# Kernel tuning notes

Measured on AMD Instinct MI355X. Metric: run time of the kernel, lower is better.

Reference implementation:

```python
import jax, jax.numpy as jnp
import numpy as np

LAMBDA = 25.0
MU = 25.0
NU = 1.0
ALPHA = 0.25
EPS = 1e-4
NUM_MATCHES = (20, 4)


def _cdist(x, y):
    # x: (B, L1, C), y: (B, L2, C) -> (B, L1, L2) euclidean distances
    x2 = jnp.sum(x * x, axis=-1)[..., :, None]
    y2 = jnp.sum(y * y, axis=-1)[..., None, :]
    d2 = x2 + y2 - 2.0 * jnp.einsum('blc,bmc->blm', x, y)
    return jnp.sqrt(jnp.maximum(d2, 0.0))


def _nearest_neighbors(input_maps, candidate_maps, distances, num_matches):
    # For each input location, its nearest candidate; then keep the
    # num_matches input locations with smallest NN distance, in original order.
    nn_dist = jnp.min(distances, axis=-1)    # (B, L1)
    nn_idx = jnp.argmin(distances, axis=-1)  # (B, L1)
    _, sel = jax.lax.top_k(-nn_dist, num_matches)  # (B, M) smallest distances
    sel = jnp.sort(sel, axis=1)  # restore original ordering of positions
    filtered_input = jnp.take_along_axis(input_maps, sel[..., None], axis=1)
    nn_sel = jnp.take_along_axis(nn_idx, sel, axis=1)
    filtered_candidate = jnp.take_along_axis(candidate_maps, nn_sel[..., None], axis=1)
    return filtered_input, filtered_candidate


def _mse(a, b):
    return jnp.mean((a - b) ** 2)


def _vicreg_loss(z_a, z_b):
    inv_loss = _mse(z_a, z_b)

    def var_loss(z):
        std = jnp.sqrt(jnp.var(z, axis=0, ddof=1) + EPS)
        return jnp.mean(jax.nn.relu(1.0 - std))

    def cov_loss(z):
        n, d = z.shape
        zc = z - jnp.mean(z, axis=0)
        cov = (zc.T @ zc) / (n - 1)
        off = cov - jnp.diag(jnp.diag(cov))
        return jnp.sum(off ** 2) / d

    v = 0.5 * (var_loss(z_a) + var_loss(z_b))
    c = cov_loss(z_a) + cov_loss(z_b)
    return LAMBDA * inv_loss + MU * v + NU * c


def _local_loss(z_global, z_local, grid_global, grid_local):
    B = z_global.shape[0]
    zg = z_global.reshape(B, -1, z_global.shape[-1])   # (B, Lg, C)
    zl = z_local.reshape(B, -1, z_local.shape[-1])     # (B, Ll, C)

    inv_loss = 0.0
    # feature-space NN
    gf, gn = _nearest_neighbors(zg, zl, _cdist(zg, zl), NUM_MATCHES[0])
    lf, ln = _nearest_neighbors(zl, zg, _cdist(zl, zg), NUM_MATCHES[1])
    inv_loss = inv_loss + (_mse(gf, gn) / 2 + _mse(lf, ln) / 2)

    # grid-space NN (distances from grids, gather from feature maps)
    gg = grid_global.reshape(B, -1, 2)
    gl = grid_local.reshape(B, -1, 2)
    gf, gn = _nearest_neighbors(zg, zl, _cdist(gg, gl), NUM_MATCHES[0])
    lf, ln = _nearest_neighbors(zl, zg, _cdist(gl, gg), NUM_MATCHES[1])
    inv_loss = inv_loss + (_mse(gf, gn) / 2 + _mse(lf, ln) / 2)

    return LAMBDA * inv_loss


def setup_inputs() -> dict:
    key = jax.random.key(0)
    ks = jax.random.split(key, 6)
    B, D, C = 32, 8192, 512
    return {
        'z_global': jax.random.normal(ks[0], (B, D), jnp.float32),
        'z_local': jax.random.normal(ks[1], (B, D), jnp.float32),
        'z_global_local_features': jax.random.normal(ks[2], (B, 24, 24, C), jnp.float32),
        'z_local_local_features': jax.random.normal(ks[3], (B, 16, 16, C), jnp.float32),
        'grid_global': jax.random.uniform(ks[4], (B, 24, 24, 2), jnp.float32),
        'grid_local': jax.random.uniform(ks[5], (B, 16, 16, 2), jnp.float32),
    }


def reference(z_global, z_local, z_global_local_features, z_local_local_features, grid_global, grid_local):
    global_loss = _vicreg_loss(z_global, z_local)
    local_loss = _local_loss(z_global_local_features, z_local_local_features, grid_global, grid_local)
    return ALPHA * global_loss + (1.0 - ALPHA) * local_loss
```

## Files before the change

kernel.cpp:

```cpp
#include <hip/hip_runtime.h>
#include <hip/hip_bf16.h>

#define BATCH 32
#define DZ    8192
#define LG    576
#define LL    256
#define CH    512

#define OFF_S      0
#define OFF_BSUM   8192
#define OFF_SELSUM 9472
#define OFF_DONE   10496
#define OFF_NG     10560
#define OFF_NL     84288
#define OFF_ROWNN  117056
#define OFF_COLNN  264512
#define OFF_ABF    330048
#define OFF_BBF    19204416
#define WS_NEED    27593024

typedef __attribute__((ext_vector_type(8))) short bf16x8;
typedef __attribute__((ext_vector_type(4))) float f32x4;

__device__ __forceinline__ unsigned short f2bf(float x) {
  union { __hip_bfloat16 h; unsigned short u; } cv;
  cv.h = __float2bfloat16(x);
  return cv.u;
}

struct SelSmem {
  unsigned long long keys[LG];
  unsigned int nnm[LG];
  float cxy[2 * LG];
  unsigned int plist[40];
  unsigned int cnt;
  float fred[4];
};

template <int V>
__device__ __forceinline__ void sel_case(
    SelSmem& sm, int b,
    const float* __restrict__ zgf, const float* __restrict__ zlf,
    const float* __restrict__ gg, const float* __restrict__ gl,
    const unsigned long long* __restrict__ rowNN,
    const unsigned long long* __restrict__ colNN,
    double* __restrict__ selsum) {
  constexpr bool GDIR = (V == 0 || V == 2);
  constexpr int L1 = GDIR ? LG : LL;
  constexpr int L2 = GDIR ? LL : LG;
  constexpr int M  = GDIR ? 20 : 4;
  constexpr int NR = (L1 + 255) / 256;
  const float* fin  = GDIR ? zgf + (size_t)b * LG * CH : zlf + (size_t)b * LL * CH;
  const float* fcan = GDIR ? zlf + (size_t)b * LL * CH : zgf + (size_t)b * LG * CH;
  int tid = threadIdx.x, lane = tid & 63, wv = tid >> 6;
  if (tid == 0) sm.cnt = 0;

  if constexpr (V < 2) {
    const unsigned long long* src =
        (V == 0) ? rowNN + (size_t)b * LG : colNN + (size_t)b * LL;
    #pragma unroll
    for (int s = 0; s < NR; ++s) {
      int l = tid + s * 256;
      if (l < L1) {
        unsigned long long p = src[l];
        sm.keys[l] = (p & 0xFFFFFFFF00000000ull) | (unsigned)l;
        sm.nnm[l] = (unsigned)(p & 0xFFFFFFFFu);
      }
    }
  } else {
    const float* gin  = (V == 2) ? gg + (size_t)b * LG * 2 : gl + (size_t)b * LL * 2;
    const float* gcan = (V == 2) ? gl + (size_t)b * LL * 2 : gg + (size_t)b * LG * 2;
    #pragma unroll
    for (int s = 0; s < (2 * L2 + 255) / 256; ++s) {
      int i = tid + s * 256;
      if (i < 2 * L2) sm.cxy[i] = gcan[i];
    }
    __syncthreads();
    float x[NR], y[NR], bd[NR];
    unsigned bi[NR];
    #pragma unroll
    for (int s = 0; s < NR; ++s) {
      int l = tid + s * 256;
      x[s] = (l < L1) ? gin[2 * l] : 0.f;
      y[s] = (l < L1) ? gin[2 * l + 1] : 0.f;
      bd[s] = 3.4e38f; bi[s] = 0;
    }
    const float2* c2 = (const float2*)sm.cxy;
    for (int m2 = 0; m2 < L2; m2 += 8) {
      float2 cc[8];
      #pragma unroll
      for (int u = 0; u < 8; ++u) cc[u] = c2[m2 + u];
      #pragma unroll
      for (int u = 0; u < 8; ++u)
        #pragma unroll
        for (int s = 0; s < NR; ++s) {
          float dx = x[s] - cc[u].x, dy = y[s] - cc[u].y;
          float d2 = dx * dx + dy * dy;
          if (d2 < bd[s]) { bd[s] = d2; bi[s] = (unsigned)(m2 + u); }
        }
    }
    #pragma unroll
    for (int s = 0; s < NR; ++s) {
      int l = tid + s * 256;
      if (l < L1) {
        sm.keys[l] = ((unsigned long long)__float_as_uint(bd[s]) << 32) | (unsigned)l;
        sm.nnm[l] = bi[s];
      }
    }
  }
  __syncthreads();

  unsigned long long myk[NR];
  int rk[NR];
  #pragma unroll
  for (int s = 0; s < NR; ++s) {
    int l = tid + s * 256;
    myk[s] = (l < L1) ? sm.keys[l] : ~0ull;
    rk[s] = 0;
  }
  for (int j = 0; j < L1; j += 8) {
    unsigned long long kk[8];
    #pragma unroll
    for (int u = 0; u < 8; ++u) kk[u] = sm.keys[j + u];
    #pragma unroll
    for (int u = 0; u < 8; ++u)
      #pragma unroll
      for (int s = 0; s < NR; ++s) rk[s] += (kk[u] < myk[s]) ? 1 : 0;
  }
  #pragma unroll
  for (int s = 0; s < NR; ++s) {
    int l = tid + s * 256;
    if (l < L1 && rk[s] < M) {
      unsigned slot = atomicAdd(&sm.cnt, 1u);
      sm.plist[2 * slot] = (unsigned)l;
      sm.plist[2 * slot + 1] = sm.nnm[l];
    }
  }
  __syncthreads();

  float part = 0.f;
  #pragma unroll
  for (int rr = 0; rr < M / 4; ++rr) {
    int r = wv + rr * 4;
    const float4* a4 = (const float4*)(fin + (size_t)sm.plist[2 * r] * CH);
    const float4* c4 = (const float4*)(fcan + (size_t)sm.plist[2 * r + 1] * CH);
    float4 xa = a4[lane * 2], xb = a4[lane * 2 + 1];
    float4 ya = c4[lane * 2], yb = c4[lane * 2 + 1];
    float d0 = xa.x - ya.x, d1 = xa.y - ya.y, d2 = xa.z - ya.z, d3 = xa.w - ya.w;
    float d4 = xb.x - yb.x, d5 = xb.y - yb.y, d6 = xb.z - yb.z, d7 = xb.w - yb.w;
    part += d0 * d0 + d1 * d1 + d2 * d2 + d3 * d3 +
            d4 * d4 + d5 * d5 + d6 * d6 + d7 * d7;
  }
  for (int s = 32; s; s >>= 1) part += __shfl_down(part, s);
  if (lane == 0) sm.fred[wv] = part;
  __syncthreads();
  if (tid == 0)
    selsum[V * 32 + b] = (double)(sm.fred[0] + sm.fred[1] + sm.fred[2] + sm.fred[3]);
}

__global__ __launch_bounds__(256) void k_front(
    const float* __restrict__ za, const float* __restrict__ zb,
    const float* __restrict__ zgf, const float* __restrict__ zlf,
    const float* __restrict__ gg, const float* __restrict__ gl,
    double* __restrict__ bsum, float* __restrict__ S,
    unsigned short* __restrict__ Abf, unsigned short* __restrict__ Bbf,
    float* __restrict__ ng, float* __restrict__ nl,
    unsigned long long* __restrict__ nnInit,
    double* __restrict__ selsum, unsigned* __restrict__ done, int do_bf16) {
  __shared__ float sred[4][8];
  __shared__ SelSmem sm;
  int tid = threadIdx.x, lane = tid & 63, wv = tid >> 6;
  int blk = blockIdx.x;

  if (blk < 64) {
    if (blk == 0 && tid == 0) *done = 0u;
    int b = blk & 31;
    if (blk >> 5)
      sel_case<3>(sm, b, zgf, zlf, gg, gl, nnInit, nnInit, selsum);
    else
      sel_case<2>(sm, b, zgf, zlf, gg, gl, nnInit, nnInit, selsum);
  } else if (blk < 96) {
    int sblk = blk - 64;
    int i = sblk * 256 + tid;
    float sa = 0.f, qa = 0.f, sb = 0.f, qb = 0.f, si = 0.f;
    #pragma unroll 8
    for (int b = 0; b < BATCH; ++b) {
      float va = za[(size_t)b * DZ + i];
      float vb = zb[(size_t)b * DZ + i];
      sa += va; qa += va * va;
      sb += vb; qb += vb * vb;
      float d = va - vb; si += d * d;
    }
    float ssa = qa - sa * sa * (1.f / 32.f);
    float ssb = qb - sb * sb * (1.f / 32.f);
    float v0 = si;
    float v1 = fmaxf(0.f, 1.f - sqrtf(ssa * (1.f / 31.f) + 1e-4f));
    float v2 = fmaxf(0.f, 1.f - sqrtf(ssb * (1.f / 31.f) + 1e-4f));
    float v3 = ssa * ssa, v4 = ssb * ssb;
    for (int off = 32; off; off >>= 1) {
      v0 += __shfl_down(v0, off); v1 += __shfl_down(v1, off);
      v2 += __shfl_down(v2, off); v3 += __shfl_down(v3, off);
      v4 += __shfl_down(v4, off);
    }
    if (lane == 0) {
      sred[wv][0] = v0; sred[wv][1] = v1; sred[wv][2] = v2;
      sred[wv][3] = v3; sred[wv][4] = v4;
    }
    __syncthreads();
    if (tid < 5)
      bsum[sblk * 5 + tid] =
          (double)(sred[0][tid] + sred[1][tid] + sred[2][tid] + sred[3][tid]);
  } else if (blk < 1152) {
    int e = blk - 96;
    int zi = e >= 528; if (zi) e -= 528;
    const float* z = zi ? zb : za;
    float* Sz = S + zi * 1024;
    int p = 0, rem = e;
    while (rem >= 32 - p) { rem -= 32 - p; ++p; }
    int q = p + rem;
    const float4* zp = (const float4*)(z + (size_t)p * DZ);
    const float4* zq = (const float4*)(z + (size_t)q * DZ);
    float s = 0.f;
    #pragma unroll
    for (int ii = 0; ii < 8; ++ii) {
      int i = tid + ii * 256;
      float4 a = zp[i], b = zq[i];
      s += a.x * b.x + a.y * b.y + a.z * b.z + a.w * b.w;
    }
    for (int off = 32; off; off >>= 1) s += __shfl_down(s, off);
    if (lane == 0) sred[wv][0] = s;
    __syncthreads();
    if (tid == 0) {
      float r = sred[0][0] + sred[1][0] + sred[2][0] + sred[3][0];
      Sz[p * 32 + q] = r;
      if (p != q) Sz[q * 32 + p] = r;
    }
  } else {
    int row = (blk - 1152) * 4 + wv;
    if (lane == 0) nnInit[row] = ~0ull;
    const float* src; unsigned short* dst; float* nrm;
    if (row < BATCH * LG) {
      src = zgf + (size_t)row * CH; dst = Abf + (size_t)row * CH; nrm = ng + row;
    } else {
      int rr = row - BATCH * LG;
      src = zlf + (size_t)rr * CH; dst = Bbf + (size_t)rr * CH; nrm = nl + rr;
    }
    const float4* s4 = (const float4*)src;
    float4 v0 = s4[lane * 2], v1 = s4[lane * 2 + 1];
    float ss = v0.x * v0.x + v0.y * v0.y + v0.z * v0.z + v0.w * v0.w +
               v1.x * v1.x + v1.y * v1.y + v1.z * v1.z + v1.w * v1.w;
    if (do_bf16) {
      union { unsigned short h[8]; uint4 u; } pk;
      pk.h[0] = f2bf(v0.x); pk.h[1] = f2bf(v0.y); pk.h[2] = f2bf(v0.z); pk.h[3] = f2bf(v0.w);
      pk.h[4] = f2bf(v1.x); pk.h[5] = f2bf(v1.y); pk.h[6] = f2bf(v1.z); pk.h[7] = f2bf(v1.w);
      *(uint4*)(dst + lane * 8) = pk.u;
    }
    for (int off = 32; off; off >>= 1) ss += __shfl_down(ss, off);
    if (lane == 0) *nrm = ss;
  }
}

__global__ __launch_bounds__(256) void k_feat_mfma(
    const unsigned short* __restrict__ Abf, const unsigned short* __restrict__ Bbf,
    const float* __restrict__ ng, const float* __restrict__ nl,
    unsigned long long* __restrict__ rowNN, unsigned long long* __restrict__ colNN) {
  const int b = blockIdx.z;
  const int row0 = blockIdx.x * 64;
  const int col0 = blockIdx.y * 64;
  const int tid = threadIdx.x;
  const int wave = tid >> 6, lane = tid & 63;
  const int m16 = lane & 15, quad = lane >> 4;
  const int wm = wave >> 1, wn = wave & 1;

  __shared__ unsigned short As[64][72];
  __shared__ unsigned short Bs[64][72];

  const unsigned short* Ag = Abf + ((size_t)(b * LG + row0)) * CH;
  const unsigned short* Bg = Bbf + ((size_t)(b * LL + col0)) * CH;

  const int sr = tid >> 2;
  const int sq = tid & 3;

  f32x4 acc[2][2] = {};

  for (int k0 = 0; k0 < CH; k0 += 64) {
    uint4 a0 = *(const uint4*)(Ag + (size_t)sr * CH + k0 + sq * 16);
    uint4 a1 = *(const uint4*)(Ag + (size_t)sr * CH + k0 + sq * 16 + 8);
    uint4 b0 = *(const uint4*)(Bg + (size_t)sr * CH + k0 + sq * 16);
    uint4 b1 = *(const uint4*)(Bg + (size_t)sr * CH + k0 + sq * 16 + 8);
    __syncthreads();
    *(uint4*)&As[sr][sq * 16] = a0; *(uint4*)&As[sr][sq * 16 + 8] = a1;
    *(uint4*)&Bs[sr][sq * 16] = b0; *(uint4*)&Bs[sr][sq * 16 + 8] = b1;
    __syncthreads();
    #pragma unroll
    for (int kk = 0; kk < 64; kk += 32) {
      bf16x8 af0 = *(const bf16x8*)&As[wm * 32 + m16][kk + quad * 8];
      bf16x8 af1 = *(const bf16x8*)&As[wm * 32 + 16 + m16][kk + quad * 8];
      bf16x8 bf0 = *(const bf16x8*)&Bs[wn * 32 + m16][kk + quad * 8];
      bf16x8 bf1 = *(const bf16x8*)&Bs[wn * 32 + 16 + m16][kk + quad * 8];
      acc[0][0] = __builtin_amdgcn_mfma_f32_16x16x32_bf16(af0, bf0, acc[0][0], 0, 0, 0);
      acc[0][1] = __builtin_amdgcn_mfma_f32_16x16x32_bf16(af0, bf1, acc[0][1], 0, 0, 0);
      acc[1][0] = __builtin_amdgcn_mfma_f32_16x16x32_bf16(af1, bf0, acc[1][0], 0, 0, 0);
      acc[1][1] = __builtin_amdgcn_mfma_f32_16x16x32_bf16(af1, bf1, acc[1][1], 0, 0, 0);
    }
  }

  float na[2][4], nb[2];
  #pragma unroll
  for (int i = 0; i < 2; ++i)
    #pragma unroll
    for (int r = 0; r < 4; ++r)
      na[i][r] = ng[b * LG + row0 + wm * 32 + i * 16 + quad * 4 + r];
  #pragma unroll
  for (int j = 0; j < 2; ++j)
    nb[j] = nl[b * LL + col0 + wn * 32 + j * 16 + m16];

  #pragma unroll
  for (int i = 0; i < 2; ++i) {
    #pragma unroll
    for (int r = 0; r < 4; ++r) {
      float d0 = fmaxf(na[i][r] + nb[0] - 2.f * acc[i][0][r], 0.f);
      float d1 = fmaxf(na[i][r] + nb[1] - 2.f * acc[i][1][r], 0.f);
      unsigned c0 = (unsigned)(col0 + wn * 32 + m16);
      unsigned long long p0 = (((unsigned long long)__float_as_uint(d0)) << 32) | c0;
      unsigned long long p1 = (((unsigned long long)__float_as_uint(d1)) << 32) | (c0 + 16);
      unsigned long long p = p0 < p1 ? p0 : p1;
      #pragma unroll
      for (int s = 1; s < 16; s <<= 1) {
        unsigned long long q = __shfl_xor(p, s);
        p = q < p ? q : p;
      }
      if (m16 == 0)
        atomicMin(&rowNN[(size_t)b * LG + row0 + wm * 32 + i * 16 + quad * 4 + r], p);
    }
  }
  #pragma unroll
  for (int j = 0; j < 2; ++j) {
    unsigned long long p = ~0ull;
    #pragma unroll
    for (int i = 0; i < 2; ++i) {
      #pragma unroll
      for (int r = 0; r < 4; ++r) {
        float d = fmaxf(na[i][r] + nb[j] - 2.f * acc[i][j][r], 0.f);
        unsigned rg = (unsigned)(row0 + wm * 32 + i * 16 + quad * 4 + r);
        unsigned long long pr = (((unsigned long long)__float_as_uint(d)) << 32) | rg;
        p = pr < p ? pr : p;
      }
    }
    unsigned long long q = __shfl_xor(p, 16); p = q < p ? q : p;
    q = __shfl_xor(p, 32); p = q < p ? q : p;
    if (quad == 0)
      atomicMin(&colNN[(size_t)b * LL + col0 + wn * 32 + j * 16 + m16], p);
  }
}

__global__ __launch_bounds__(256) void k_feat_nn(
    const float* __restrict__ zgf, const float* __restrict__ zlf,
    const float* __restrict__ ng, const float* __restrict__ nl,
    unsigned long long* __restrict__ rowNN, unsigned long long* __restrict__ colNN) {
  const int b = blockIdx.z;
  const int row0 = blockIdx.x * 64;
  const int col0 = blockIdx.y * 128;
  const int tid = threadIdx.x;
  const int tx = tid & 15, ty = tid >> 4;
  __shared__ float As[64][20];
  __shared__ float Bs[128][20];
  __shared__ float Ds[64][130];
  const float* Ag = zgf + ((size_t)b * LG + row0) * CH;
  const float* Bg = zlf + ((size_t)b * LL + col0) * CH;
  float acc[4][8];
  #pragma unroll
  for (int i = 0; i < 4; ++i)
    #pragma unroll
    for (int j = 0; j < 8; ++j) acc[i][j] = 0.f;
  const int ar = tid >> 2;
  const int ak = (tid & 3) * 4;
  for (int k0 = 0; k0 < CH; k0 += 16) {
    float4 av  = *(const float4*)(Ag + (size_t)ar * CH + k0 + ak);
    float4 bv0 = *(const float4*)(Bg + (size_t)ar * CH + k0 + ak);
    float4 bv1 = *(const float4*)(Bg + (size_t)(ar + 64) * CH + k0 + ak);
    __syncthreads();
    *(float4*)&As[ar][ak] = av;
    *(float4*)&Bs[ar][ak] = bv0;
    *(float4*)&Bs[ar + 64][ak] = bv1;
    __syncthreads();
    #pragma unroll
    for (int k = 0; k < 16; ++k) {
      float a0 = As[ty][k], a1 = As[ty + 16][k], a2 = As[ty + 32][k], a3 = As[ty + 48][k];
      float bv[8];
      #pragma unroll
      for (int j = 0; j < 8; ++j) bv[j] = Bs[tx + 16 * j][k];
      #pragma unroll
      for (int j = 0; j < 8; ++j) {
        acc[0][j] += a0 * bv[j]; acc[1][j] += a1 * bv[j];
        acc[2][j] += a2 * bv[j]; acc[3][j] += a3 * bv[j];
      }
    }
  }
  float ngr[4], nlc[8];
  #pragma unroll
  for (int i = 0; i < 4; ++i) ngr[i] = ng[b * LG + row0 + ty + 16 * i];
  #pragma unroll
  for (int j = 0; j < 8; ++j) nlc[j] = nl[b * LL + col0 + tx + 16 * j];
  #pragma unroll
  for (int i = 0; i < 4; ++i)
    #pragma unroll
    for (int j = 0; j < 8; ++j)
      Ds[ty + 16 * i][tx + 16 * j] = fmaxf(ngr[i] + nlc[j] - 2.f * acc[i][j], 0.f);
  __syncthreads();
  if (tid < 64) {
    unsigned long long best = ~0ull;
    for (int c = 0; c < 128; ++c) {
      unsigned long long p =
          ((unsigned long long)__float_as_uint(Ds[tid][c]) << 32) | (unsigned)(col0 + c);
      best = p < best ? p : best;
    }
    atomicMin(&rowNN[(size_t)b * LG + row0 + tid], best);
  } else if (tid < 192) {
    int c = tid - 64;
    unsigned long long best = ~0ull;
    for (int r = 0; r < 64; ++r) {
      unsigned long long p =
          ((unsigned long long)__float_as_uint(Ds[r][c]) << 32) | (unsigned)(row0 + r);
      best = p < best ? p : best;
    }
    atomicMin(&colNN[(size_t)b * LL + col0 + c], best);
  }
}

__global__ __launch_bounds__(256) void k_sel(
    const float* __restrict__ zgf, const float* __restrict__ zlf,
    const float* __restrict__ gg, const float* __restrict__ gl,
    const unsigned long long* __restrict__ rowNN,
    const unsigned long long* __restrict__ colNN,
    double* __restrict__ selsum, const double* __restrict__ bsum,
    const float* __restrict__ S, unsigned* __restrict__ done,
    float* __restrict__ out) {
  __shared__ SelSmem sm;
  int b = blockIdx.x;
  if (blockIdx.y == 0)
    sel_case<0>(sm, b, zgf, zlf, gg, gl, rowNN, colNN, selsum);
  else
    sel_case<1>(sm, b, zgf, zlf, gg, gl, rowNN, colNN, selsum);

  __shared__ unsigned isLast;
  __shared__ float t[2][32];
  __shared__ double sacc[5];
  __shared__ double smf[4];
  __shared__ double totred[2];
  int tid = threadIdx.x, lane = tid & 63, wv = tid >> 6;
  if (tid == 0) {
    __threadfence();
    unsigned old = __hip_atomic_fetch_add(done, 1u, __ATOMIC_ACQ_REL,
                                          __HIP_MEMORY_SCOPE_AGENT);
    isLast = (old == 63u) ? 1u : 0u;
  }
  __syncthreads();
  if (isLast) {
    __threadfence();
    if (tid < 64) {
      int zi = tid >> 5, p = tid & 31;
      float tp = 0.f;
      for (int bb = 0; bb < 32; ++bb) tp += S[zi * 1024 + p * 32 + bb];
      t[zi][p] = tp * (1.f / 32.f);
    } else if (tid < 69) {
      int k = tid - 64;
      double s = 0.0;
      for (int blk = 0; blk < 32; ++blk) s += bsum[blk * 5 + k];
      sacc[k] = s;
    } else if (tid >= 72 && tid < 76) {
      int v = tid - 72;
      double s = 0.0;
      for (int bb = 0; bb < 32; ++bb) s += selsum[v * 32 + bb];
      smf[v] = s;
    }
    __syncthreads();
    if (wv < 2) {
      int zi = wv;
      float u = 0.f;
      for (int bb = 0; bb < 32; ++bb) u += t[zi][bb];
      u *= (1.f / 32.f);
      double s = 0.0;
      for (int e = lane; e < 1024; e += 64) {
        int p = e >> 5, q = e & 31;
        float G = S[zi * 1024 + e] - t[zi][p] - t[zi][q] + u;
        s += (double)G * (double)G;
      }
      for (int off = 32; off; off >>= 1) s += __shfl_down(s, off);
      if (lane == 0) totred[zi] = s;
    }
    __syncthreads();
    if (tid == 0) {
      double inv_g = sacc[0] / (32.0 * 8192.0);
      double v = 0.5 * (sacc[1] + sacc[2]) / 8192.0;
      double c = (totred[0] - sacc[3] + totred[1] - sacc[4]) / (961.0 * 8192.0);
      double gloss = 25.0 * inv_g + 25.0 * v + c;
      double mfg = smf[0] / (32.0 * 20.0 * 512.0);
      double mfl = smf[1] / (32.0 * 4.0 * 512.0);
      double mgg = smf[2] / (32.0 * 20.0 * 512.0);
      double mgl = smf[3] / (32.0 * 4.0 * 512.0);
      double lloss = 25.0 * (0.5 * (mfg + mfl) + 0.5 * (mgg + mgl));
      out[0] = (float)(0.25 * gloss + 0.75 * lloss);
    }
  }
}

extern "C" void kernel_launch(void* const* d_in, const int* in_sizes, int n_in,
                              void* d_out, int out_size, void* d_ws, size_t ws_size,
                              hipStream_t stream) {
  const float* zg  = (const float*)d_in[0];
  const float* zl  = (const float*)d_in[1];
  const float* zgf = (const float*)d_in[2];
  const float* zlf = (const float*)d_in[3];
  const float* gg  = (const float*)d_in[4];
  const float* glo = (const float*)d_in[5];

  char* ws = (char*)d_ws;
  float* S       = (float*)(ws + OFF_S);
  double* bsum   = (double*)(ws + OFF_BSUM);
  double* selsum = (double*)(ws + OFF_SELSUM);
  unsigned* done = (unsigned*)(ws + OFF_DONE);
  float* ng = (float*)(ws + OFF_NG);
  float* nl = (float*)(ws + OFF_NL);
  unsigned long long* rowNN = (unsigned long long*)(ws + OFF_ROWNN);
  unsigned long long* colNN = (unsigned long long*)(ws + OFF_COLNN);
  unsigned short* Abf = (unsigned short*)(ws + OFF_ABF);
  unsigned short* Bbf = (unsigned short*)(ws + OFF_BBF);

  int do_bf16 = (ws_size >= WS_NEED) ? 1 : 0;

  k_front<<<7808, 256, 0, stream>>>(zg, zl, zgf, zlf, gg, glo, bsum, S,
                                    Abf, Bbf, ng, nl, rowNN, selsum, done, do_bf16);
  if (do_bf16) {
    k_feat_mfma<<<dim3(LG / 64, LL / 64, BATCH), 256, 0, stream>>>(
        Abf, Bbf, ng, nl, rowNN, colNN);
  } else {
    k_feat_nn<<<dim3(LG / 64, LL / 128, BATCH), 256, 0, stream>>>(
        zgf, zlf, ng, nl, rowNN, colNN);
  }
  k_sel<<<dim3(BATCH, 2), 256, 0, stream>>>(zgf, zlf, gg, glo, rowNN, colNN,
                                            selsum, bsum, S, done, (float*)d_out);
}
```

Measured before the change: 171.3 us.

## Fuse bf16 conversion and norms into MFMA kernel and merge selection via per-batch counters

The front kernel no longer converts the feature maps to bf16 or computes row norms. That removes writing and rereading a large bf16 staging buffer and the separate norm arrays. The MFMA distance kernel now reads fp32 features directly, converts them to bf16 on the fly, and accumulates the squared norms during tiling. The separate selection kernel is folded in: the last tile block of each batch, found with per-batch atomic counters, runs the feature-space selection, and a final counter picks the block that reduces the loss. This cuts one launch and a lot of memory traffic, at the cost of redundant fp32 loads and conversions per tile and serialized tail work in the last blocks.

```diff
diff --git a/kernel.cpp b/kernel.cpp
--- a/kernel.cpp
+++ b/kernel.cpp
@@ -10,14 +10,9 @@
 #define OFF_S      0
 #define OFF_BSUM   8192
 #define OFF_SELSUM 9472
-#define OFF_DONE   10496
-#define OFF_NG     10560
-#define OFF_NL     84288
-#define OFF_ROWNN  117056
-#define OFF_COLNN  264512
-#define OFF_ABF    330048
-#define OFF_BBF    19204416
-#define WS_NEED    27593024
+#define OFF_CNT    10496
+#define OFF_ROWNN  10752
+#define OFF_COLNN  158208
 
 typedef __attribute__((ext_vector_type(8))) short bf16x8;
 typedef __attribute__((ext_vector_type(4))) float f32x4;
@@ -26,6 +21,19 @@
   union { __hip_bfloat16 h; unsigned short u; } cv;
   cv.h = __float2bfloat16(x);
   return cv.u;
+}
+
+__device__ __forceinline__ unsigned long long ld_nn(const unsigned long long* p) {
+  return __hip_atomic_load(p, __ATOMIC_RELAXED, __HIP_MEMORY_SCOPE_AGENT);
+}
+__device__ __forceinline__ void st_sum(double* p, double v) {
+  __hip_atomic_store((unsigned long long*)p,
+                     (unsigned long long)__double_as_longlong(v),
+                     __ATOMIC_RELAXED, __HIP_MEMORY_SCOPE_AGENT);
+}
+__device__ __forceinline__ double ld_sum(const double* p) {
+  return __longlong_as_double((long long)__hip_atomic_load(
+      (const unsigned long long*)p, __ATOMIC_RELAXED, __HIP_MEMORY_SCOPE_AGENT));
 }
 
 struct SelSmem {
@@ -62,7 +70,7 @@
     for (int s = 0; s < NR; ++s) {
       int l = tid + s * 256;
       if (l < L1) {
-        unsigned long long p = src[l];
+        unsigned long long p = ld_nn(&src[l]);
         sm.keys[l] = (p & 0xFFFFFFFF00000000ull) | (unsigned)l;
         sm.nnm[l] = (unsigned)(p & 0xFFFFFFFFu);
       }
@@ -155,7 +163,9 @@
   if (lane == 0) sm.fred[wv] = part;
   __syncthreads();
   if (tid == 0)
-    selsum[V * 32 + b] = (double)(sm.fred[0] + sm.fred[1] + sm.fred[2] + sm.fred[3]);
+    st_sum(&selsum[V * 32 + b],
+           (double)(sm.fred[0] + sm.fred[1] + sm.fred[2] + sm.fred[3]));
+  __syncthreads();
 }
 
 __global__ __launch_bounds__(256) void k_front(
@@ -163,17 +173,15 @@
     const float* __restrict__ zgf, const float* __restrict__ zlf,
     const float* __restrict__ gg, const float* __restrict__ gl,
     double* __restrict__ bsum, float* __restrict__ S,
-    unsigned short* __restrict__ Abf, unsigned short* __restrict__ Bbf,
-    float* __restrict__ ng, float* __restrict__ nl,
     unsigned long long* __restrict__ nnInit,
-    double* __restrict__ selsum, unsigned* __restrict__ done, int do_bf16) {
+    double* __restrict__ selsum, unsigned* __restrict__ cnt) {
   __shared__ float sred[4][8];
   __shared__ SelSmem sm;
   int tid = threadIdx.x, lane = tid & 63, wv = tid >> 6;
   int blk = blockIdx.x;
 
   if (blk < 64) {
-    if (blk == 0 && tid == 0) *done = 0u;
+    if (blk == 0 && tid < 33) cnt[tid] = 0u;
     int b = blk & 31;
     if (blk >> 5)
       sel_case<3>(sm, b, zgf, zlf, gg, gl, nnInit, nnInit, selsum);
@@ -236,34 +244,18 @@
       if (p != q) Sz[q * 32 + p] = r;
     }
   } else {
-    int row = (blk - 1152) * 4 + wv;
-    if (lane == 0) nnInit[row] = ~0ull;
-    const float* src; unsigned short* dst; float* nrm;
-    if (row < BATCH * LG) {
-      src = zgf + (size_t)row * CH; dst = Abf + (size_t)row * CH; nrm = ng + row;
-    } else {
-      int rr = row - BATCH * LG;
-      src = zlf + (size_t)rr * CH; dst = Bbf + (size_t)rr * CH; nrm = nl + rr;
-    }
-    const float4* s4 = (const float4*)src;
-    float4 v0 = s4[lane * 2], v1 = s4[lane * 2 + 1];
-    float ss = v0.x * v0.x + v0.y * v0.y + v0.z * v0.z + v0.w * v0.w +
-               v1.x * v1.x + v1.y * v1.y + v1.z * v1.z + v1.w * v1.w;
-    if (do_bf16) {
-      union { unsigned short h[8]; uint4 u; } pk;
-      pk.h[0] = f2bf(v0.x); pk.h[1] = f2bf(v0.y); pk.h[2] = f2bf(v0.z); pk.h[3] = f2bf(v0.w);
-      pk.h[4] = f2bf(v1.x); pk.h[5] = f2bf(v1.y); pk.h[6] = f2bf(v1.z); pk.h[7] = f2bf(v1.w);
-      *(uint4*)(dst + lane * 8) = pk.u;
-    }
-    for (int off = 32; off; off >>= 1) ss += __shfl_down(ss, off);
-    if (lane == 0) *nrm = ss;
-  }
-}
-
-__global__ __launch_bounds__(256) void k_feat_mfma(
-    const unsigned short* __restrict__ Abf, const unsigned short* __restrict__ Bbf,
-    const float* __restrict__ ng, const float* __restrict__ nl,
-    unsigned long long* __restrict__ rowNN, unsigned long long* __restrict__ colNN) {
+    int idx = (blk - 1152) * 256 + tid;
+    nnInit[idx] = ~0ull;
+  }
+}
+
+__global__ __launch_bounds__(256) void k_mfma_sel(
+    const float* __restrict__ zgf, const float* __restrict__ zlf,
+    const float* __restrict__ gg, const float* __restrict__ gl,
+    unsigned long long* __restrict__ rowNN, unsigned long long* __restrict__ colNN,
+    double* __restrict__ selsum, const double* __restrict__ bsum,
+    const float* __restrict__ S, unsigned* __restrict__ cnt,
+    float* __restrict__ out) {
   const int b = blockIdx.z;
   const int row0 = blockIdx.x * 64;
   const int col0 = blockIdx.y * 64;
@@ -272,32 +264,68 @@
   const int m16 = lane & 15, quad = lane >> 4;
   const int wm = wave >> 1, wn = wave & 1;
 
-  __shared__ unsigned short As[64][72];
-  __shared__ unsigned short Bs[64][72];
-
-  const unsigned short* Ag = Abf + ((size_t)(b * LG + row0)) * CH;
-  const unsigned short* Bg = Bbf + ((size_t)(b * LL + col0)) * CH;
+  __shared__ union {
+    struct {
+      unsigned short As[64][72];
+      unsigned short Bs[64][72];
+      float nA[64];
+      float nB[64];
+    } m;
+    SelSmem s;
+  } u;
+  __shared__ unsigned tflag, fflag;
+  __shared__ float t[2][32];
+  __shared__ double sacc[5], smf[4], totred[2];
+
+  const float* Ag = zgf + ((size_t)(b * LG + row0)) * CH;
+  const float* Bg = zlf + ((size_t)(b * LL + col0)) * CH;
 
   const int sr = tid >> 2;
   const int sq = tid & 3;
 
   f32x4 acc[2][2] = {};
+  float nra = 0.f, nrb = 0.f;
 
   for (int k0 = 0; k0 < CH; k0 += 64) {
-    uint4 a0 = *(const uint4*)(Ag + (size_t)sr * CH + k0 + sq * 16);
-    uint4 a1 = *(const uint4*)(Ag + (size_t)sr * CH + k0 + sq * 16 + 8);
-    uint4 b0 = *(const uint4*)(Bg + (size_t)sr * CH + k0 + sq * 16);
-    uint4 b1 = *(const uint4*)(Bg + (size_t)sr * CH + k0 + sq * 16 + 8);
-    __syncthreads();
-    *(uint4*)&As[sr][sq * 16] = a0; *(uint4*)&As[sr][sq * 16 + 8] = a1;
-    *(uint4*)&Bs[sr][sq * 16] = b0; *(uint4*)&Bs[sr][sq * 16 + 8] = b1;
+    const float* ap = Ag + (size_t)sr * CH + k0 + sq * 16;
+    const float* bp = Bg + (size_t)sr * CH + k0 + sq * 16;
+    float4 a0 = *(const float4*)(ap);
+    float4 a1 = *(const float4*)(ap + 4);
+    float4 a2 = *(const float4*)(ap + 8);
+    float4 a3 = *(const float4*)(ap + 12);
+    float4 b0 = *(const float4*)(bp);
+    float4 b1 = *(const float4*)(bp + 4);
+    float4 b2 = *(const float4*)(bp + 8);
+    float4 b3 = *(const float4*)(bp + 12);
+    nra += a0.x * a0.x + a0.y * a0.y + a0.z * a0.z + a0.w * a0.w +
+           a1.x * a1.x + a1.y * a1.y + a1.z * a1.z + a1.w * a1.w +
+           a2.x * a2.x + a2.y * a2.y + a2.z * a2.z + a2.w * a2.w +
+           a3.x * a3.x + a3.y * a3.y + a3.z * a3.z + a3.w * a3.w;
+    nrb += b0.x * b0.x + b0.y * b0.y + b0.z * b0.z + b0.w * b0.w +
+           b1.x * b1.x + b1.y * b1.y + b1.z * b1.z + b1.w * b1.w +
+           b2.x * b2.x + b2.y * b2.y + b2.z * b2.z + b2.w * b2.w +
+           b3.x * b3.x + b3.y * b3.y + b3.z * b3.z + b3.w * b3.w;
+    union { unsigned short h[8]; uint4 q; } pa0, pa1, pb0, pb1;
+    pa0.h[0] = f2bf(a0.x); pa0.h[1] = f2bf(a0.y); pa0.h[2] = f2bf(a0.z); pa0.h[3] = f2bf(a0.w);
+    pa0.h[4] = f2bf(a1.x); pa0.h[5] = f2bf(a1.y); pa0.h[6] = f2bf(a1.z); pa0.h[7] = f2bf(a1.w);
+    pa1.h[0] = f2bf(a2.x); pa1.h[1] = f2bf(a2.y); pa1.h[2] = f2bf(a2.z); pa1.h[3] = f2bf(a2.w);
+    pa1.h[4] = f2bf(a3.x); pa1.h[5] = f2bf(a3.y); pa1.h[6] = f2bf(a3.z); pa1.h[7] = f2bf(a3.w);
+    pb0.h[0] = f2bf(b0.x); pb0.h[1] = f2bf(b0.y); pb0.h[2] = f2bf(b0.z); pb0.h[3] = f2bf(b0.w);
+    pb0.h[4] = f2bf(b1.x); pb0.h[5] = f2bf(b1.y); pb0.h[6] = f2bf(b1.z); pb0.h[7] = f2bf(b1.w);
+    pb1.h[0] = f2bf(b2.x); pb1.h[1] = f2bf(b2.y); pb1.h[2] = f2bf(b2.z); pb1.h[3] = f2bf(b2.w);
+    pb1.h[4] = f2bf(b3.x); pb1.h[5] = f2bf(b3.y); pb1.h[6] = f2bf(b3.z); pb1.h[7] = f2bf(b3.w);
+    __syncthreads();
+    *(uint4*)&u.m.As[sr][sq * 16] = pa0.q;
+    *(uint4*)&u.m.As[sr][sq * 16 + 8] = pa1.q;
+    *(uint4*)&u.m.Bs[sr][sq * 16] = pb0.q;
+    *(uint4*)&u.m.Bs[sr][sq * 16 + 8] = pb1.q;
     __syncthreads();
     #pragma unroll
     for (int kk = 0; kk < 64; kk += 32) {
-      bf16x8 af0 = *(const bf16x8*)&As[wm * 32 + m16][kk + quad * 8];
-      bf16x8 af1 = *(const bf16x8*)&As[wm * 32 + 16 + m16][kk + quad * 8];
-      bf16x8 bf0 = *(const bf16x8*)&Bs[wn * 32 + m16][kk + quad * 8];
-      bf16x8 bf1 = *(const bf16x8*)&Bs[wn * 32 + 16 + m16][kk + quad * 8];
+      bf16x8 af0 = *(const bf16x8*)&u.m.As[wm * 32 + m16][kk + quad * 8];
+      bf16x8 af1 = *(const bf16x8*)&u.m.As[wm * 32 + 16 + m16][kk + quad * 8];
+      bf16x8 bf0 = *(const bf16x8*)&u.m.Bs[wn * 32 + m16][kk + quad * 8];
+      bf16x8 bf1 = *(const bf16x8*)&u.m.Bs[wn * 32 + 16 + m16][kk + quad * 8];
       acc[0][0] = __builtin_amdgcn_mfma_f32_16x16x32_bf16(af0, bf0, acc[0][0], 0, 0, 0);
       acc[0][1] = __builtin_amdgcn_mfma_f32_16x16x32_bf16(af0, bf1, acc[0][1], 0, 0, 0);
       acc[1][0] = __builtin_amdgcn_mfma_f32_16x16x32_bf16(af1, bf0, acc[1][0], 0, 0, 0);
@@ -305,22 +333,27 @@
     }
   }
 
-  float na[2][4], nb[2];
+  nra += __shfl_xor(nra, 1); nra += __shfl_xor(nra, 2);
+  nrb += __shfl_xor(nrb, 1); nrb += __shfl_xor(nrb, 2);
+  if (sq == 0) { u.m.nA[sr] = nra; u.m.nB[sr] = nrb; }
+  __syncthreads();
+
+  float na[2][4], nb2[2];
   #pragma unroll
   for (int i = 0; i < 2; ++i)
     #pragma unroll
     for (int r = 0; r < 4; ++r)
-      na[i][r] = ng[b * LG + row0 + wm * 32 + i * 16 + quad * 4 + r];
+      na[i][r] = u.m.nA[wm * 32 + i * 16 + quad * 4 + r];
   #pragma unroll
   for (int j = 0; j < 2; ++j)
-    nb[j] = nl[b * LL + col0 + wn * 32 + j * 16 + m16];
+    nb2[j] = u.m.nB[wn * 32 + j * 16 + m16];
 
   #pragma unroll
   for (int i = 0; i < 2; ++i) {
     #pragma unroll
     for (int r = 0; r < 4; ++r) {
-      float d0 = fmaxf(na[i][r] + nb[0] - 2.f * acc[i][0][r], 0.f);
-      float d1 = fmaxf(na[i][r] + nb[1] - 2.f * acc[i][1][r], 0.f);
+      float d0 = fmaxf(na[i][r] + nb2[0] - 2.f * acc[i][0][r], 0.f);
+      float d1 = fmaxf(na[i][r] + nb2[1] - 2.f * acc[i][1][r], 0.f);
       unsigned c0 = (unsigned)(col0 + wn * 32 + m16);
       unsigned long long p0 = (((unsigned long long)__float_as_uint(d0)) << 32) | c0;
       unsigned long long p1 = (((unsigned long long)__float_as_uint(d1)) << 32) | (c0 + 16);
@@ -341,7 +374,7 @@
     for (int i = 0; i < 2; ++i) {
       #pragma unroll
       for (int r = 0; r < 4; ++r) {
-        float d = fmaxf(na[i][r] + nb[j] - 2.f * acc[i][j][r], 0.f);
+        float d = fmaxf(na[i][r] + nb2[j] - 2.f * acc[i][j][r], 0.f);
         unsigned rg = (unsigned)(row0 + wm * 32 + i * 16 + quad * 4 + r);
         unsigned long long pr = (((unsigned long long)__float_as_uint(d)) << 32) | rg;
         p = pr < p ? pr : p;
@@ -352,155 +385,72 @@
     if (quad == 0)
       atomicMin(&colNN[(size_t)b * LL + col0 + wn * 32 + j * 16 + m16], p);
   }
-}
-
-__global__ __launch_bounds__(256) void k_feat_nn(
-    const float* __restrict__ zgf, const float* __restrict__ zlf,
-    const float* __restrict__ ng, const float* __restrict__ nl,
-    unsigned long long* __restrict__ rowNN, unsigned long long* __restrict__ colNN) {
-  const int b = blockIdx.z;
-  const int row0 = blockIdx.x * 64;
-  const int col0 = blockIdx.y * 128;
-  const int tid = threadIdx.x;
-  const int tx = tid & 15, ty = tid >> 4;
-  __shared__ float As[64][20];
-  __shared__ float Bs[128][20];
-  __shared__ float Ds[64][130];
-  const float* Ag = zgf + ((size_t)b * LG + row0) * CH;
-  const float* Bg = zlf + ((size_t)b * LL + col0) * CH;
-  float acc[4][8];
-  #pragma unroll
-  for (int i = 0; i < 4; ++i)
-    #pragma unroll
-    for (int j = 0; j < 8; ++j) acc[i][j] = 0.f;
-  const int ar = tid >> 2;
-  const int ak = (tid & 3) * 4;
-  for (int k0 = 0; k0 < CH; k0 += 16) {
-    float4 av  = *(const float4*)(Ag + (size_t)ar * CH + k0 + ak);
-    float4 bv0 = *(const float4*)(Bg + (size_t)ar * CH + k0 + ak);
-    float4 bv1 = *(const float4*)(Bg + (size_t)(ar + 64) * CH + k0 + ak);
-    __syncthreads();
-    *(float4*)&As[ar][ak] = av;
-    *(float4*)&Bs[ar][ak] = bv0;
-    *(float4*)&Bs[ar + 64][ak] = bv1;
-    __syncthreads();
-    #pragma unroll
-    for (int k = 0; k < 16; ++k) {
-      float a0 = As[ty][k], a1 = As[ty + 16][k], a2 = As[ty + 32][k], a3 = As[ty + 48][k];
-      float bv[8];
-      #pragma unroll
-      for (int j = 0; j < 8; ++j) bv[j] = Bs[tx + 16 * j][k];
-      #pragma unroll
-      for (int j = 0; j < 8; ++j) {
-        acc[0][j] += a0 * bv[j]; acc[1][j] += a1 * bv[j];
-        acc[2][j] += a2 * bv[j]; acc[3][j] += a3 * bv[j];
-      }
-    }
-  }
-  float ngr[4], nlc[8];
-  #pragma unroll
-  for (int i = 0; i < 4; ++i) ngr[i] = ng[b * LG + row0 + ty + 16 * i];
-  #pragma unroll
-  for (int j = 0; j < 8; ++j) nlc[j] = nl[b * LL + col0 + tx + 16 * j];
-  #pragma unroll
-  for (int i = 0; i < 4; ++i)
-    #pragma unroll
-    for (int j = 0; j < 8; ++j)
-      Ds[ty + 16 * i][tx + 16 * j] = fmaxf(ngr[i] + nlc[j] - 2.f * acc[i][j], 0.f);
-  __syncthreads();
-  if (tid < 64) {
-    unsigned long long best = ~0ull;
-    for (int c = 0; c < 128; ++c) {
-      unsigned long long p =
-          ((unsigned long long)__float_as_uint(Ds[tid][c]) << 32) | (unsigned)(col0 + c);
-      best = p < best ? p : best;
-    }
-    atomicMin(&rowNN[(size_t)b * LG + row0 + tid], best);
-  } else if (tid < 192) {
-    int c = tid - 64;
-    unsigned long long best = ~0ull;
-    for (int r = 0; r < 64; ++r) {
-      unsigned long long p =
-          ((unsigned long long)__float_as_uint(Ds[r][c]) << 32) | (unsigned)(row0 + r);
-      best = p < best ? p : best;
-    }
-    atomicMin(&colNN[(size_t)b * LL + col0 + c], best);
-  }
-}
-
-__global__ __launch_bounds__(256) void k_sel(
-    const float* __restrict__ zgf, const float* __restrict__ zlf,
-    const float* __restrict__ gg, const float* __restrict__ gl,
-    const unsigned long long* __restrict__ rowNN,
-    const unsigned long long* __restrict__ colNN,
-    double* __restrict__ selsum, const double* __restrict__ bsum,
-    const float* __restrict__ S, unsigned* __restrict__ done,
-    float* __restrict__ out) {
-  __shared__ SelSmem sm;
-  int b = blockIdx.x;
-  if (blockIdx.y == 0)
-    sel_case<0>(sm, b, zgf, zlf, gg, gl, rowNN, colNN, selsum);
-  else
-    sel_case<1>(sm, b, zgf, zlf, gg, gl, rowNN, colNN, selsum);
-
-  __shared__ unsigned isLast;
-  __shared__ float t[2][32];
-  __shared__ double sacc[5];
-  __shared__ double smf[4];
-  __shared__ double totred[2];
-  int tid = threadIdx.x, lane = tid & 63, wv = tid >> 6;
+
+  __threadfence();
+  __syncthreads();
   if (tid == 0) {
+    unsigned old = __hip_atomic_fetch_add(&cnt[b], 1u, __ATOMIC_ACQ_REL,
+                                          __HIP_MEMORY_SCOPE_AGENT);
+    tflag = (old == 35u) ? 1u : 0u;
+  }
+  __syncthreads();
+  if (tflag) {
     __threadfence();
-    unsigned old = __hip_atomic_fetch_add(done, 1u, __ATOMIC_ACQ_REL,
-                                          __HIP_MEMORY_SCOPE_AGENT);
-    isLast = (old == 63u) ? 1u : 0u;
-  }
-  __syncthreads();
-  if (isLast) {
+    sel_case<0>(u.s, b, zgf, zlf, gg, gl, rowNN, colNN, selsum);
+    sel_case<1>(u.s, b, zgf, zlf, gg, gl, rowNN, colNN, selsum);
     __threadfence();
-    if (tid < 64) {
-      int zi = tid >> 5, p = tid & 31;
-      float tp = 0.f;
-      for (int bb = 0; bb < 32; ++bb) tp += S[zi * 1024 + p * 32 + bb];
-      t[zi][p] = tp * (1.f / 32.f);
-    } else if (tid < 69) {
-      int k = tid - 64;
-      double s = 0.0;
-      for (int blk = 0; blk < 32; ++blk) s += bsum[blk * 5 + k];
-      sacc[k] = s;
-    } else if (tid >= 72 && tid < 76) {
-      int v = tid - 72;
-      double s = 0.0;
-      for (int bb = 0; bb < 32; ++bb) s += selsum[v * 32 + bb];
-      smf[v] = s;
-    }
-    __syncthreads();
-    if (wv < 2) {
-      int zi = wv;
-      float u = 0.f;
-      for (int bb = 0; bb < 32; ++bb) u += t[zi][bb];
-      u *= (1.f / 32.f);
-      double s = 0.0;
-      for (int e = lane; e < 1024; e += 64) {
-        int p = e >> 5, q = e & 31;
-        float G = S[zi * 1024 + e] - t[zi][p] - t[zi][q] + u;
-        s += (double)G * (double)G;
-      }
-      for (int off = 32; off; off >>= 1) s += __shfl_down(s, off);
-      if (lane == 0) totred[zi] = s;
-    }
-    __syncthreads();
     if (tid == 0) {
-      double inv_g = sacc[0] / (32.0 * 8192.0);
-      double v = 0.5 * (sacc[1] + sacc[2]) / 8192.0;
-      double c = (totred[0] - sacc[3] + totred[1] - sacc[4]) / (961.0 * 8192.0);
-      double gloss = 25.0 * inv_g + 25.0 * v + c;
-      double mfg = smf[0] / (32.0 * 20.0 * 512.0);
-      double mfl = smf[1] / (32.0 * 4.0 * 512.0);
-      double mgg = smf[2] / (32.0 * 20.0 * 512.0);
-      double mgl = smf[3] / (32.0 * 4.0 * 512.0);
-      double lloss = 25.0 * (0.5 * (mfg + mfl) + 0.5 * (mgg + mgl));
-      out[0] = (float)(0.25 * gloss + 0.75 * lloss);
+      unsigned old2 = __hip_atomic_fetch_add(&cnt[32], 1u, __ATOMIC_ACQ_REL,
+                                             __HIP_MEMORY_SCOPE_AGENT);
+      fflag = (old2 == 31u) ? 1u : 0u;
+    }
+    __syncthreads();
+    if (fflag) {
+      __threadfence();
+      if (tid < 64) {
+        int zi = tid >> 5, p = tid & 31;
+        float tp = 0.f;
+        for (int bb = 0; bb < 32; ++bb) tp += S[zi * 1024 + p * 32 + bb];
+        t[zi][p] = tp * (1.f / 32.f);
+      } else if (tid < 69) {
+        int k = tid - 64;
+        double s = 0.0;
+        for (int blk = 0; blk < 32; ++blk) s += bsum[blk * 5 + k];
+        sacc[k] = s;
+      } else if (tid >= 72 && tid < 76) {
+        int v = tid - 72;
+        double s = 0.0;
+        for (int bb = 0; bb < 32; ++bb) s += ld_sum(&selsum[v * 32 + bb]);
+        smf[v] = s;
+      }
+      __syncthreads();
+      if (wave < 2) {
+        int zi = wave;
+        float uu = 0.f;
+        for (int bb = 0; bb < 32; ++bb) uu += t[zi][bb];
+        uu *= (1.f / 32.f);
+        double s = 0.0;
+        for (int e = lane; e < 1024; e += 64) {
+          int p = e >> 5, q = e & 31;
+          float G = S[zi * 1024 + e] - t[zi][p] - t[zi][q] + uu;
+          s += (double)G * (double)G;
+        }
+        for (int off = 32; off; off >>= 1) s += __shfl_down(s, off);
+        if (lane == 0) totred[zi] = s;
+      }
+      __syncthreads();
+      if (tid == 0) {
+        double inv_g = sacc[0] / (32.0 * 8192.0);
+        double v = 0.5 * (sacc[1] + sacc[2]) / 8192.0;
+        double c = (totred[0] - sacc[3] + totred[1] - sacc[4]) / (961.0 * 8192.0);
+        double gloss = 25.0 * inv_g + 25.0 * v + c;
+        double mfg = smf[0] / (32.0 * 20.0 * 512.0);
+        double mfl = smf[1] / (32.0 * 4.0 * 512.0);
+        double mgg = smf[2] / (32.0 * 20.0 * 512.0);
+        double mgl = smf[3] / (32.0 * 4.0 * 512.0);
+        double lloss = 25.0 * (0.5 * (mfg + mfl) + 0.5 * (mgg + mgl));
+        out[0] = (float)(0.25 * gloss + 0.75 * lloss);
+      }
     }
   }
 }
@@ -519,25 +469,12 @@
   float* S       = (float*)(ws + OFF_S);
   double* bsum   = (double*)(ws + OFF_BSUM);
   double* selsum = (double*)(ws + OFF_SELSUM);
-  unsigned* done = (unsigned*)(ws + OFF_DONE);
-  float* ng = (float*)(ws + OFF_NG);
-  float* nl = (float*)(ws + OFF_NL);
+  unsigned* cnt  = (unsigned*)(ws + OFF_CNT);
   unsigned long long* rowNN = (unsigned long long*)(ws + OFF_ROWNN);
   unsigned long long* colNN = (unsigned long long*)(ws + OFF_COLNN);
-  unsigned short* Abf = (unsigned short*)(ws + OFF_ABF);
-  unsigned short* Bbf = (unsigned short*)(ws + OFF_BBF);
-
-  int do_bf16 = (ws_size >= WS_NEED) ? 1 : 0;
-
-  k_front<<<7808, 256, 0, stream>>>(zg, zl, zgf, zlf, gg, glo, bsum, S,
-                                    Abf, Bbf, ng, nl, rowNN, selsum, done, do_bf16);
-  if (do_bf16) {
-    k_feat_mfma<<<dim3(LG / 64, LL / 64, BATCH), 256, 0, stream>>>(
-        Abf, Bbf, ng, nl, rowNN, colNN);
-  } else {
-    k_feat_nn<<<dim3(LG / 64, LL / 128, BATCH), 256, 0, stream>>>(
-        zgf, zlf, ng, nl, rowNN, colNN);
-  }
-  k_sel<<<dim3(BATCH, 2), 256, 0, stream>>>(zgf, zlf, gg, glo, rowNN, colNN,
-                                            selsum, bsum, S, done, (float*)d_out);
-}
+
+  k_front<<<1256, 256, 0, stream>>>(zg, zl, zgf, zlf, gg, glo,
+                                    bsum, S, rowNN, selsum, cnt);
+  k_mfma_sel<<<dim3(LG / 64, LL / 64, BATCH), 256, 0, stream>>>(
+      zgf, zlf, gg, glo, rowNN, colNN, selsum, bsum, S, cnt, (float*)d_out);
+}
```

After: 353.3 us. 2.06x slower.
